# Kernel tuning notes

Hardware: AMD Instinct MI355X
Metric: run time of the kernel (lower is better)

The kernel has to match this reference:

```python
import jax, jax.numpy as jnp
import numpy as np

TEMPERATURE = 0.05


def setup_inputs() -> dict:
    key = jax.random.key(0)
    k1, k2 = jax.random.split(key)
    B, D = 4096, 1024
    # scale 0.1 keeps pairwise distances O(3) so the original exp(-d/T) is sane
    text_embeddings = 0.1 * jax.random.normal(k1, (B, D), dtype=jnp.float32)
    image_embeddings = 0.1 * jax.random.normal(k2, (B, D), dtype=jnp.float32)
    positive_pairs = jnp.arange(B, dtype=jnp.int32)  # unused by the loss body
    return {
        "text_embeddings": text_embeddings,
        "image_embeddings": image_embeddings,
        "positive_pairs": positive_pairs,
    }


def _pairwise_l2(t, m):
    # ||t_i - m_j|| via GEMM expansion; [B, B]
    sq = (
        jnp.sum(t * t, axis=1, keepdims=True)
        + jnp.sum(m * m, axis=1)[None, :]
        - 2.0 * (t @ m.T)
    )
    return jnp.sqrt(jnp.maximum(sq, 0.0))


def reference(text_embeddings, image_embeddings, positive_pairs):
    # loss_i = -log( exp(-d_ii/T) / sum_{j != i} exp(-d_ij/T) )
    #        = logsumexp_{j != i}(-d_ij/T) + d_ii/T   (exact same math, stable)
    dist = _pairwise_l2(text_embeddings, image_embeddings)  # [B, B]
    logits = -dist / TEMPERATURE
    diag = jnp.diagonal(logits)  # log numerator per row
    B = logits.shape[0]
    eye = jnp.eye(B, dtype=bool)
    masked = jnp.where(eye, -jnp.inf, logits)  # exclude self-term from denom
    lse = jax.nn.logsumexp(masked, axis=1)
    return jnp.mean(lse - diag)
```

## Files before the change

### kernel.cpp

```cpp
#include <hip/hip_runtime.h>
#include <math.h>


#define NB 4096
#define ND 1024
#define LSE_BIAS 90.0f
#define A2 28.85390082f
#define C2 129.8425537f
#define LN2 0.6931471805599453f
#define SCALE1 0x7F7F7F7Fu

typedef int v8i __attribute__((ext_vector_type(8)));
typedef int int4v __attribute__((ext_vector_type(4)));
typedef float v16f __attribute__((ext_vector_type(16)));

__device__ inline void gload_lds16(const unsigned char* g, unsigned char* l) {
  __builtin_amdgcn_global_load_lds(
      (const __attribute__((address_space(1))) unsigned int*)g,
      (__attribute__((address_space(3))) unsigned int*)l, 16, 0, 0);
}

__global__ void prep_kernel(const float* __restrict__ T, const float* __restrict__ M,
                            unsigned char* __restrict__ t8, unsigned char* __restrict__ m8,
                            float* __restrict__ tn, float* __restrict__ mn,
                            float* __restrict__ out) {
  int row = blockIdx.x;
  if (row == 0 && threadIdx.x == 0) out[0] = 0.0f;
  const float* src;
  unsigned char* dst;
  float* nout;
  int r;
  if (row < NB) { src = T; dst = t8; nout = tn; r = row; }
  else          { src = M; dst = m8; nout = mn; r = row - NB; }
  float4 v = ((const float4*)(src + (size_t)r * ND))[threadIdx.x];
  float s = v.x * v.x + v.y * v.y + v.z * v.z + v.w * v.w;
  int p = __builtin_amdgcn_cvt_pk_fp8_f32(v.x, v.y, 0, false);
  p = __builtin_amdgcn_cvt_pk_fp8_f32(v.z, v.w, p, true);
  ((int*)(dst + (size_t)r * ND))[threadIdx.x] = p;
  for (int off = 32; off; off >>= 1) s += __shfl_xor(s, off);
  __shared__ float wsum[4];
  if ((threadIdx.x & 63) == 0) wsum[threadIdx.x >> 6] = s;
  __syncthreads();
  if (threadIdx.x == 0) nout[r] = wsum[0] + wsum[1] + wsum[2] + wsum[3];
}

__launch_bounds__(512, 2)
__global__ void gemm_lse_kernel(const unsigned char* __restrict__ t8,
                                const unsigned char* __restrict__ m8,
                                const float* __restrict__ tn, const float* __restrict__ mn,
                                float* __restrict__ part_s, float* __restrict__ diag) {
  __shared__ unsigned char A0[256 * 128];
  __shared__ unsigned char A1[256 * 128];
  __shared__ unsigned char B0[256 * 128];
  __shared__ unsigned char B1[256 * 128];
  int b = blockIdx.x;
  int region = b & 7, idx = b >> 3;
  int rt = ((region >> 2) << 3) | (idx & 7);
  int ct = ((region & 3) << 2) | (idx >> 3);
  int tid = threadIdx.x;
  int wave = tid >> 6, lane = tid & 63;
  int hb = lane >> 5, l31 = lane & 31;
  int wr = wave >> 2, wc = wave & 3;

  v16f acc[4][2] = {};

  int l3 = lane >> 3;
  int gc = (lane & 7) ^ l3;
  const unsigned char* gA0 = t8 + (size_t)(rt * 256 + wave * 8 + l3) * ND + gc * 16;
  const unsigned char* gB0 = m8 + (size_t)(ct * 256 + wc * 8 + l3) * ND + gc * 16;

  int sw = l31 & 7;
  int arow = (wr * 128 + l31) * 128;
  int brow = (wc * 64 + l31) * 128;

#define ISSUE_A(DST, I, KOFF)                                                   \
  do {                                                                          \
    gload_lds16(gA0 + (size_t)((I) * 64 * ND) + (KOFF),                         \
                DST + ((I) * 64 + wave * 8) * 128);                             \
    gload_lds16(gA0 + (size_t)(((I) * 64 + 128) * ND) + (KOFF),                 \
                DST + ((I) * 64 + 128 + wave * 8) * 128);                       \
  } while (0)

#define ISSUE_B(DST, J, KOFF)                                                   \
  do {                                                                          \
    gload_lds16(gB0 + (size_t)((wr * 64 + (J) * 32) * ND) + (KOFF),             \
                DST + (wr * 64 + (J) * 32 + wc * 8) * 128);                     \
    gload_lds16(gB0 + (size_t)(((2 + wr) * 64 + (J) * 32) * ND) + (KOFF),       \
                DST + ((2 + wr) * 64 + (J) * 32 + wc * 8) * 128);               \
  } while (0)

#define PHASE(SA, SB, I, J, ISSUE_STMT, DO_WAIT)                                \
  do {                                                                          \
    v8i af_[2][2], bf_[2];                                                      \
    _Pragma("unroll") for (int ks = 0; ks < 2; ++ks) {                          \
      int q16 = ((ks * 4 + 2 * hb) ^ sw) * 16;                                  \
      _Pragma("unroll") for (int f = 0; f < 2; ++f) {                           \
        int4v x0 = *(const int4v*)&SA[arow + ((I) * 2 + f) * 4096 + q16];       \
        int4v x1 = *(const int4v*)&SA[arow + ((I) * 2 + f) * 4096 + (q16 ^ 16)];\
        af_[ks][f] = (v8i){x0.x, x0.y, x0.z, x0.w, x1.x, x1.y, x1.z, x1.w};     \
      }                                                                         \
      int4v y0 = *(const int4v*)&SB[brow + (J) * 4096 + q16];                   \
      int4v y1 = *(const int4v*)&SB[brow + (J) * 4096 + (q16 ^ 16)];            \
      bf_[ks] = (v8i){y0.x, y0.y, y0.z, y0.w, y1.x, y1.y, y1.z, y1.w};          \
    }                                                                           \
    ISSUE_STMT;                                                                 \
    if (DO_WAIT) asm volatile("s_waitcnt vmcnt(4)" ::: "memory");               \
    __builtin_amdgcn_s_barrier();                                               \
    __builtin_amdgcn_s_setprio(1);                                              \
    _Pragma("unroll") for (int ks = 0; ks < 2; ++ks)                            \
      _Pragma("unroll") for (int f = 0; f < 2; ++f)                             \
        acc[(I) * 2 + f][J] = __builtin_amdgcn_mfma_scale_f32_32x32x64_f8f6f4(  \
            af_[ks][f], bf_[ks], acc[(I) * 2 + f][J], 0, 0, 0, SCALE1, 0, SCALE1); \
    __builtin_amdgcn_s_setprio(0);                                              \
    __builtin_amdgcn_s_barrier();                                               \
  } while (0)

  ISSUE_A(A0, 0, 0);
  ISSUE_A(A0, 1, 0);
  ISSUE_B(B0, 0, 0);
  ISSUE_B(B0, 1, 0);
  ISSUE_A(A1, 0, 128);
  ISSUE_B(B1, 0, 128);
  asm volatile("s_waitcnt vmcnt(4)" ::: "memory");
  __builtin_amdgcn_s_barrier();

#pragma unroll 1
  for (int kt2 = 0; kt2 < 4; ++kt2) {
    int k1 = (2 * kt2 + 1) * 128;
    int k2 = ((2 * kt2 + 2) * 128) & (ND - 1);
    int k3 = ((2 * kt2 + 3) * 128) & (ND - 1);
    PHASE(A0, B0, 0, 0, ISSUE_A(A1, 1, k1), 0);
    PHASE(A0, B0, 0, 1, ISSUE_B(B1, 1, k1), 0);
    PHASE(A0, B0, 1, 0, ISSUE_A(A0, 0, k2), 0);
    PHASE(A0, B0, 1, 1, ISSUE_B(B0, 0, k2), 1);
    PHASE(A1, B1, 0, 0, ISSUE_A(A0, 1, k2), 0);
    PHASE(A1, B1, 0, 1, ISSUE_B(B0, 1, k2), 0);
    PHASE(A1, B1, 1, 0, ISSUE_A(A1, 0, k3), 0);
    PHASE(A1, B1, 1, 1, ISSUE_B(B1, 0, k3), 1);
  }
#undef PHASE
#undef ISSUE_A
#undef ISSUE_B
  asm volatile("s_waitcnt vmcnt(0)" ::: "memory");
  __builtin_amdgcn_s_barrier();

  int chunk = ct * 4 + wc;
  bool diagblk = (rt == ct);
  float mnv[2];
#pragma unroll
  for (int fc = 0; fc < 2; ++fc) mnv[fc] = mn[ct * 256 + wc * 64 + fc * 32 + l31];
#pragma unroll
  for (int fr = 0; fr < 4; ++fr) {
#pragma unroll
    for (int reg = 0; reg < 16; ++reg) {
      int row = (reg & 3) + 8 * (reg >> 2) + 4 * hb;
      int grow = rt * 256 + wr * 128 + fr * 32 + row;
      float tnr = tn[grow];
      float s = 0.0f;
#pragma unroll
      for (int fc = 0; fc < 2; ++fc) {
        float sq = fmaxf(fmaf(-2.0f, acc[fr][fc][reg], tnr + mnv[fc]), 0.0f);
        float dr = __builtin_amdgcn_sqrtf(sq);
        float e = __builtin_amdgcn_exp2f(fmaf(dr, -A2, C2));
        if (diagblk) {
          int gcol = ct * 256 + wc * 64 + fc * 32 + l31;
          if (grow == gcol) {
            diag[grow] = -20.0f * dr;
            e = 0.0f;
          }
        }
        s += e;
      }
      for (int m = 16; m; m >>= 1) s += __shfl_xor(s, m);
      if (l31 == 0) part_s[(size_t)grow * 64 + chunk] = s;
    }
  }
}

__global__ void combine_kernel(const float* __restrict__ part_s,
                               const float* __restrict__ diag, float* __restrict__ out) {
  int row = blockIdx.x * 256 + threadIdx.x;
  const float* ps = part_s + (size_t)row * 64;
  float S = 0.0f;
#pragma unroll 8
  for (int c = 0; c < 64; ++c) S += ps[c];
  float loss = (LN2 * __builtin_amdgcn_logf(S) - LSE_BIAS) - diag[row];
  for (int off = 32; off; off >>= 1) loss += __shfl_xor(loss, off);
  __shared__ float wsum[4];
  if ((threadIdx.x & 63) == 0) wsum[threadIdx.x >> 6] = loss;
  __syncthreads();
  if (threadIdx.x == 0)
    atomicAdd(out, (wsum[0] + wsum[1] + wsum[2] + wsum[3]) * (1.0f / (float)NB));
}

extern "C" void kernel_launch(void* const* d_in, const int* in_sizes, int n_in,
                              void* d_out, int out_size, void* d_ws, size_t ws_size,
                              hipStream_t stream) {
  const float* T = (const float*)d_in[0];
  const float* M = (const float*)d_in[1];
  float* out = (float*)d_out;

  unsigned char* t8 = (unsigned char*)d_ws;
  unsigned char* m8 = t8 + (size_t)NB * ND;
  float* fbase = (float*)(m8 + (size_t)NB * ND);
  float* tn = fbase;
  float* mn = tn + NB;
  float* diag = mn + NB;
  float* part_s = diag + NB;

  prep_kernel<<<2 * NB, 256, 0, stream>>>(T, M, t8, m8, tn, mn, out);
  gemm_lse_kernel<<<(NB / 256) * (NB / 256), 512, 0, stream>>>(t8, m8, tn, mn, part_s, diag);
  combine_kernel<<<NB / 256, 256, 0, stream>>>(part_s, diag, out);
}
```

Measured before the change: 126.1 us.

## Software-pipeline LDS fragment reads one phase ahead of MFMA compute

Restructures the FP8 GEMM main loop so the A/B register fragments for the next phase are read from LDS before the current phase's MFMAs, using double-buffered fragment registers (aX/aY, bP/bQ). Global-to-LDS issues move after the MFMAs, and the waitcnt values are retuned to match. Fragments are reused across adjacent phases, so some phases skip LDS reads entirely. The aim is to hide LDS latency behind matrix math and cut redundant fragment loads. The cost is higher register pressure and subtler barrier/vmcnt correctness for buffer reuse.

```diff
diff --git a/kernel.cpp b/kernel.cpp
--- a/kernel.cpp
+++ b/kernel.cpp
@@ -18,6 +18,12 @@
   __builtin_amdgcn_global_load_lds(
       (const __attribute__((address_space(1))) unsigned int*)g,
       (__attribute__((address_space(3))) unsigned int*)l, 16, 0, 0);
+}
+
+__device__ inline v8i ldfrag(const unsigned char* p0, const unsigned char* p1) {
+  int4v x0 = *(const int4v*)p0;
+  int4v x1 = *(const int4v*)p1;
+  return (v8i){x0.x, x0.y, x0.z, x0.w, x1.x, x1.y, x1.z, x1.w};
 }
 
 __global__ void prep_kernel(const float* __restrict__ T, const float* __restrict__ M,
@@ -72,6 +78,8 @@
   int sw = l31 & 7;
   int arow = (wr * 128 + l31) * 128;
   int brow = (wc * 64 + l31) * 128;
+  int q0 = ((2 * hb) ^ sw) * 16;
+  int q1 = ((4 + 2 * hb) ^ sw) * 16;
 
 #define ISSUE_A(DST, I, KOFF)                                                   \
   do {                                                                          \
@@ -89,31 +97,38 @@
                 DST + ((2 + wr) * 64 + (J) * 32 + wc * 8) * 128);               \
   } while (0)
 
-#define PHASE(SA, SB, I, J, ISSUE_STMT, DO_WAIT)                                \
+#define AFRAG(SA, I, f, q) \
+  ldfrag(&SA[arow + ((I) * 2 + (f)) * 4096 + (q)], &SA[arow + ((I) * 2 + (f)) * 4096 + ((q) ^ 16)])
+#define READ_AF(N, SA, I)                                                       \
+  N##00 = AFRAG(SA, I, 0, q0); N##01 = AFRAG(SA, I, 0, q1);                     \
+  N##10 = AFRAG(SA, I, 1, q0); N##11 = AFRAG(SA, I, 1, q1)
+#define READ_BF(N, SB, J)                                                       \
+  N##0 = ldfrag(&SB[brow + (J) * 4096 + q0], &SB[brow + (J) * 4096 + (q0 ^ 16)]); \
+  N##1 = ldfrag(&SB[brow + (J) * 4096 + q1], &SB[brow + (J) * 4096 + (q1 ^ 16)])
+
+#define MFMA4(AN, BN, I, J)                                                     \
+  acc[(I) * 2 + 0][J] = __builtin_amdgcn_mfma_scale_f32_32x32x64_f8f6f4(        \
+      AN##00, BN##0, acc[(I) * 2 + 0][J], 0, 0, 0, SCALE1, 0, SCALE1);          \
+  acc[(I) * 2 + 1][J] = __builtin_amdgcn_mfma_scale_f32_32x32x64_f8f6f4(        \
+      AN##10, BN##0, acc[(I) * 2 + 1][J], 0, 0, 0, SCALE1, 0, SCALE1);          \
+  acc[(I) * 2 + 0][J] = __builtin_amdgcn_mfma_scale_f32_32x32x64_f8f6f4(        \
+      AN##01, BN##1, acc[(I) * 2 + 0][J], 0, 0, 0, SCALE1, 0, SCALE1);          \
+  acc[(I) * 2 + 1][J] = __builtin_amdgcn_mfma_scale_f32_32x32x64_f8f6f4(        \
+      AN##11, BN##1, acc[(I) * 2 + 1][J], 0, 0, 0, SCALE1, 0, SCALE1)
+
+#define BODY(AN, BN, I, J, READS, ISSUES, WAITSTR)                              \
   do {                                                                          \
-    v8i af_[2][2], bf_[2];                                                      \
-    _Pragma("unroll") for (int ks = 0; ks < 2; ++ks) {                          \
-      int q16 = ((ks * 4 + 2 * hb) ^ sw) * 16;                                  \
-      _Pragma("unroll") for (int f = 0; f < 2; ++f) {                           \
-        int4v x0 = *(const int4v*)&SA[arow + ((I) * 2 + f) * 4096 + q16];       \
-        int4v x1 = *(const int4v*)&SA[arow + ((I) * 2 + f) * 4096 + (q16 ^ 16)];\
-        af_[ks][f] = (v8i){x0.x, x0.y, x0.z, x0.w, x1.x, x1.y, x1.z, x1.w};     \
-      }                                                                         \
-      int4v y0 = *(const int4v*)&SB[brow + (J) * 4096 + q16];                   \
-      int4v y1 = *(const int4v*)&SB[brow + (J) * 4096 + (q16 ^ 16)];            \
-      bf_[ks] = (v8i){y0.x, y0.y, y0.z, y0.w, y1.x, y1.y, y1.z, y1.w};          \
-    }                                                                           \
-    ISSUE_STMT;                                                                 \
-    if (DO_WAIT) asm volatile("s_waitcnt vmcnt(4)" ::: "memory");               \
-    __builtin_amdgcn_s_barrier();                                               \
+    READS;                                                                      \
     __builtin_amdgcn_s_setprio(1);                                              \
-    _Pragma("unroll") for (int ks = 0; ks < 2; ++ks)                            \
-      _Pragma("unroll") for (int f = 0; f < 2; ++f)                             \
-        acc[(I) * 2 + f][J] = __builtin_amdgcn_mfma_scale_f32_32x32x64_f8f6f4(  \
-            af_[ks][f], bf_[ks], acc[(I) * 2 + f][J], 0, 0, 0, SCALE1, 0, SCALE1); \
+    MFMA4(AN, BN, I, J);                                                        \
     __builtin_amdgcn_s_setprio(0);                                              \
+    ISSUES;                                                                     \
+    asm volatile("s_waitcnt " WAITSTR ::: "memory");                            \
     __builtin_amdgcn_s_barrier();                                               \
   } while (0)
+
+  v8i aX00, aX01, aX10, aX11, aY00, aY01, aY10, aY11;
+  v8i bP0, bP1, bQ0, bQ1;
 
   ISSUE_A(A0, 0, 0);
   ISSUE_A(A0, 1, 0);
@@ -123,22 +138,30 @@
   ISSUE_B(B1, 0, 128);
   asm volatile("s_waitcnt vmcnt(4)" ::: "memory");
   __builtin_amdgcn_s_barrier();
+  READ_AF(aX, A0, 0);
+  READ_BF(bP, B0, 0);
 
 #pragma unroll 1
   for (int kt2 = 0; kt2 < 4; ++kt2) {
     int k1 = (2 * kt2 + 1) * 128;
     int k2 = ((2 * kt2 + 2) * 128) & (ND - 1);
     int k3 = ((2 * kt2 + 3) * 128) & (ND - 1);
-    PHASE(A0, B0, 0, 0, ISSUE_A(A1, 1, k1), 0);
-    PHASE(A0, B0, 0, 1, ISSUE_B(B1, 1, k1), 0);
-    PHASE(A0, B0, 1, 0, ISSUE_A(A0, 0, k2), 0);
-    PHASE(A0, B0, 1, 1, ISSUE_B(B0, 0, k2), 1);
-    PHASE(A1, B1, 0, 0, ISSUE_A(A0, 1, k2), 0);
-    PHASE(A1, B1, 0, 1, ISSUE_B(B0, 1, k2), 0);
-    PHASE(A1, B1, 1, 0, ISSUE_A(A1, 0, k3), 0);
-    PHASE(A1, B1, 1, 1, ISSUE_B(B1, 0, k3), 1);
+    BODY(aX, bP, 0, 0, ({ READ_AF(aY, A0, 1); READ_BF(bQ, B0, 1); }),
+         ({ ISSUE_A(A1, 1, k1); ISSUE_B(B1, 1, k1); }), "vmcnt(8)");
+    BODY(aX, bQ, 0, 1, ({}), ({}), "vmcnt(6)");
+    BODY(aY, bP, 1, 0, ({ READ_AF(aX, A1, 0); }), ({ ISSUE_A(A0, 0, k2); }), "vmcnt(6)");
+    BODY(aY, bQ, 1, 1, ({ READ_BF(bP, B1, 0); }), ({ ISSUE_B(B0, 0, k2); }), "vmcnt(4)");
+    BODY(aX, bP, 0, 0, ({ READ_AF(aY, A1, 1); READ_BF(bQ, B1, 1); }),
+         ({ ISSUE_A(A0, 1, k2); ISSUE_B(B0, 1, k2); }), "vmcnt(8)");
+    BODY(aX, bQ, 0, 1, ({}), ({}), "vmcnt(6)");
+    BODY(aY, bP, 1, 0, ({ READ_AF(aX, A0, 0); }), ({ ISSUE_A(A1, 0, k3); }), "vmcnt(6)");
+    BODY(aY, bQ, 1, 1, ({ READ_BF(bP, B0, 0); }), ({ ISSUE_B(B1, 0, k3); }), "vmcnt(4)");
   }
-#undef PHASE
+#undef BODY
+#undef MFMA4
+#undef READ_AF
+#undef READ_BF
+#undef AFRAG
 #undef ISSUE_A
 #undef ISSUE_B
   asm volatile("s_waitcnt vmcnt(0)" ::: "memory");
```

After: 132.7 us. 1.05x slower.
